# Optimization experiments

Measured on AMD Instinct MI355X. Metric: run time of the kernel, lower is better.

The kernel has to match this reference:

```python
import jax, jax.numpy as jnp
import numpy as np

N = 50000
E = 1600000
F_IN = 128
MP_UNITS = [32, 32, 32, 32, 16, 16, 16, 16, 8, 8, 8, 8]
MLP_UNITS = [16, 16]
DELTA = 2.0


def _lin(k, fi, fo):
    kw, kb = jax.random.split(k)
    s = 1.0 / np.sqrt(fi)
    W = jax.random.uniform(kw, (fi, fo), minval=-s, maxval=s, dtype=jnp.float32)
    b = jax.random.uniform(kb, (fo,), minval=-s, maxval=s, dtype=jnp.float32)
    return W, b


def setup_inputs() -> dict:
    key = jax.random.key(0)
    ks = jax.random.split(key, 64)
    inp = {}
    inp['x'] = jax.random.normal(ks[0], (N, F_IN), dtype=jnp.float32)
    inp['edge_index'] = jax.random.randint(ks[1], (2, E), 0, N, dtype=jnp.int32)
    inp['edge_weight'] = jax.random.uniform(ks[2], (E,), dtype=jnp.float32)
    inp['Wi'], inp['bi'] = _lin(ks[3], F_IN, F_IN)
    d = F_IN
    for i, u in enumerate(MP_UNITS):
        inp['Wc%d' % i], inp['bc%d' % i] = _lin(ks[4 + i], d, u)
        d = u
    for i, u in enumerate(MLP_UNITS):
        inp['Wm%d' % i], inp['bm%d' % i] = _lin(ks[20 + i], d, u)
        d = u
    inp['Wf'], inp['bf'] = _lin(ks[30], d, 1)
    return inp


def reference(x, edge_index, edge_weight, Wi, bi,
              Wc0, bc0, Wc1, bc1, Wc2, bc2, Wc3, bc3, Wc4, bc4, Wc5, bc5,
              Wc6, bc6, Wc7, bc7, Wc8, bc8, Wc9, bc9, Wc10, bc10, Wc11, bc11,
              Wm0, bm0, Wm1, bm1, Wf, bf):
    n = x.shape[0]
    src, dst = edge_index[0], edge_index[1]
    # delta_gcn_matrix: P = (1-delta) I + delta * D^{-1/2} A D^{-1/2}
    deg = jax.ops.segment_sum(edge_weight, dst, num_segments=n)
    dinv = jnp.where(deg > 0, jax.lax.rsqrt(jnp.maximum(deg, 1e-12)), 0.0)
    w = DELTA * dinv[src] * edge_weight * dinv[dst]  # [E]
    self_w = 1.0 - DELTA

    h = x @ Wi + bi

    def conv(h, W, b):
        hw = h @ W                                        # [N, out]
        msg = hw[src] * w[:, None]                        # gather + scale [E, out]
        agg = jax.ops.segment_sum(msg, dst, num_segments=n)  # scatter-add
        return agg + self_w * hw + b                      # fold in self-loops

    convs = [(Wc0, bc0), (Wc1, bc1), (Wc2, bc2), (Wc3, bc3), (Wc4, bc4), (Wc5, bc5),
             (Wc6, bc6), (Wc7, bc7), (Wc8, bc8), (Wc9, bc9), (Wc10, bc10), (Wc11, bc11)]
    for W, b in convs:
        h = jnp.tanh(conv(h, W, b))
    for W, b in [(Wm0, bm0), (Wm1, bm1)]:
        h = jax.nn.relu(h @ W + b)
    return jnp.tanh(h @ Wf + bf)  # [N, 1]
```

## Files before the change

### kernel.cpp

```cpp
#include <hip/hip_runtime.h>


constexpr int kN = 50000;
constexpr int kE = 1600000;
constexpr float kSelfW = -1.0f;
constexpr int kCAP = 72;
constexpr int PAD_N = 50048;
constexpr int kPROWS = PAD_N / 8;
constexpr int E4  = kE / 4;
constexpr int E4B = (E4 + 255) / 256;
constexpr int NBG = (kN + 255) / 256;

typedef int      v4i __attribute__((ext_vector_type(4)));
typedef float    v4f __attribute__((ext_vector_type(4)));
typedef _Float16 h8v __attribute__((ext_vector_type(8)));

__device__ __forceinline__ int rowmap(int r) {
  return (r & 7) * kPROWS + (r >> 3);
}
__device__ __forceinline__ unsigned packcw(int col, float w) {
  _Float16 h = (_Float16)w;
  unsigned short u;
  __builtin_memcpy(&u, &h, 2);
  return (unsigned)(unsigned short)col | ((unsigned)u << 16);
}
__device__ __forceinline__ float unpw(unsigned e) {
  unsigned short u = (unsigned short)(e >> 16);
  _Float16 h;
  __builtin_memcpy(&h, &u, 2);
  return (float)h;
}
__device__ __forceinline__ float fast_tanh(float x) {
  float t = __expf(2.0f * x);
  float r = __builtin_amdgcn_rcpf(t + 1.0f);
  return 1.0f - 2.0f * r;
}

__global__ __launch_bounds__(256)
void prep(int* __restrict__ cnt, const float* __restrict__ Wi,
          const float* __restrict__ bi, const float* __restrict__ Wc0,
          float* __restrict__ Weff, float* __restrict__ beff) {
  if (blockIdx.x < 49) {
    int i = blockIdx.x * 1024 + threadIdx.x * 4;
    if (i < PAD_N) *reinterpret_cast<int4*>(cnt + i) = make_int4(0, 0, 0, 0);
  } else {
    int idx = (blockIdx.x - 49) * 256 + threadIdx.x;
    if (idx >= 129 * 32) return;
    int r = idx >> 5, j = idx & 31;
    float acc = 0.0f;
    if (r < 128) {
      for (int k = 0; k < 128; ++k) acc += Wi[r * 128 + k] * Wc0[k * 32 + j];
      Weff[r * 32 + j] = acc;
    } else {
      for (int k = 0; k < 128; ++k) acc += bi[k] * Wc0[k * 32 + j];
      beff[j] = acc;
    }
  }
}

__global__ __launch_bounds__(256)
void cnt_rank_kernel(const int* __restrict__ dst, int* __restrict__ cnt,
                     int* __restrict__ rank, int e4) {
  int i = blockIdx.x * blockDim.x + threadIdx.x;
  if (i >= e4) return;
  int4 d = reinterpret_cast<const int4*>(dst)[i];
  int4 r;
  r.x = atomicAdd(&cnt[d.x], 1);
  r.y = atomicAdd(&cnt[d.y], 1);
  r.z = atomicAdd(&cnt[d.z], 1);
  r.w = atomicAdd(&cnt[d.w], 1);
  reinterpret_cast<int4*>(rank)[i] = r;
}

__global__ __launch_bounds__(256)
void gemm0(const float* __restrict__ X, const float* __restrict__ Weff,
           const float* __restrict__ beff, _Float16* __restrict__ Y, int n) {
  __shared__ float smem[4128];
  for (int idx = threadIdx.x; idx < 128 * 32; idx += 256) {
    int j = idx >> 7, k = idx & 127;
    smem[j * 128 + k] = Weff[k * 32 + j];
  }
  if (threadIdx.x < 32) smem[4096 + threadIdx.x] = beff[threadIdx.x];
  __syncthreads();
  int row = blockIdx.x * 256 + threadIdx.x;
  if (row >= n) return;
  float acc[32];
#pragma unroll
  for (int j = 0; j < 32; ++j) acc[j] = smem[4096 + j];
  const float4* xr = reinterpret_cast<const float4*>(X + (size_t)row * 128);
  const float4* Ws4 = reinterpret_cast<const float4*>(smem);
  for (int k4 = 0; k4 < 32; ++k4) {
    float4 a = xr[k4];
#pragma unroll
    for (int j = 0; j < 32; ++j) {
      float4 wv = Ws4[j * 32 + k4];
      acc[j] += a.x * wv.x + a.y * wv.y + a.z * wv.z + a.w * wv.w;
    }
  }
  h8v* yr = reinterpret_cast<h8v*>(Y + (size_t)row * 32);
#pragma unroll
  for (int j8 = 0; j8 < 4; ++j8) {
    h8v v;
#pragma unroll
    for (int q = 0; q < 8; ++q) v[q] = (_Float16)acc[8 * j8 + q];
    yr[j8] = v;
  }
}

__global__ __launch_bounds__(256)
void build_part(const int* __restrict__ src, const int* __restrict__ dst,
                const float* __restrict__ ew, const int* __restrict__ rank,
                unsigned* __restrict__ ecw, int e4) {
  int p = blockIdx.x & 7;
  int i = (blockIdx.x >> 3) * 256 + threadIdx.x;
  if (i >= e4) return;
  v4i sv = __builtin_nontemporal_load(reinterpret_cast<const v4i*>(src) + i);
  v4i dv = __builtin_nontemporal_load(reinterpret_cast<const v4i*>(dst) + i);
  v4i rv = __builtin_nontemporal_load(reinterpret_cast<const v4i*>(rank) + i);
  v4f wv = __builtin_nontemporal_load(reinterpret_cast<const v4f*>(ew) + i);
#pragma unroll
  for (int c = 0; c < 4; ++c) {
    int d = dv[c];
    if ((d & 7) == p) {
      int r = rv[c];
      if (r < kCAP)
        ecw[(size_t)(p * kPROWS + (d >> 3)) * kCAP + r] = packcw(sv[c], wv[c]);
    }
  }
}

__global__ __launch_bounds__(256)
void deg_dinv_wave(const int* __restrict__ cnt, const unsigned* __restrict__ ecw,
                   float* __restrict__ dinv, int n) {
  int lane = threadIdx.x & 63;
  int row = blockIdx.x * 4 + (threadIdx.x >> 6);
  int deg = min(cnt[row], kCAP);
  int base = rowmap(row) * kCAP;
  float d = 0.0f;
  for (int i = lane; i < deg; i += 64) d += unpw(ecw[base + i]);
#pragma unroll
  for (int off = 32; off > 0; off >>= 1) d += __shfl_xor(d, off, 64);
  if (lane == 0) dinv[row] = (d > 0.0f) ? rsqrtf(fmaxf(d, 1e-12f)) : 0.0f;
}

__global__ __launch_bounds__(256)
void wscale_wave(const int* __restrict__ cnt, unsigned* __restrict__ ecw,
                 const float* __restrict__ dinv, int n) {
  int lane = threadIdx.x & 63;
  int row = blockIdx.x * 4 + (threadIdx.x >> 6);
  int deg = min(cnt[row], kCAP);
  int base = rowmap(row) * kCAP;
  float dr = 2.0f * dinv[row];
  for (int i = lane; i < kCAP; i += 64) {
    if (i < deg) {
      unsigned e = ecw[base + i];
      int col = e & 0xFFFFu;
      ecw[base + i] = packcw(col, dr * dinv[col] * unpw(e));
    } else {
      ecw[base + i] = 0u;
    }
  }
}

template <int DOUT, int DNEXT, bool FINAL>
__global__ __launch_bounds__(256)
void spmm_fused(const _Float16* __restrict__ HW, const int* __restrict__ cnt,
                const unsigned* __restrict__ ecw, const float* __restrict__ b,
                const float* __restrict__ Wn, void* __restrict__ Out,
                const float* __restrict__ Wm0, const float* __restrict__ bm0,
                const float* __restrict__ Wm1, const float* __restrict__ bm1,
                const float* __restrict__ Wf, const float* __restrict__ bf,
                int n) {
  constexpr int R = 32 / DOUT;
  constexpr int W = 64 / R;
  constexpr int L = DOUT / 8;
  constexpr int S = W / L;
  constexpr int WST = DNEXT + 1;
  __shared__ float smem[(DNEXT > 0) ? DOUT * WST : 448];
  if constexpr (DNEXT > 0) {
    for (int idx = threadIdx.x; idx < DOUT * DNEXT; idx += 256) {
      int k = idx / DNEXT, j = idx - k * DNEXT;
      smem[k * WST + j] = Wn[idx];
    }
    __syncthreads();
  }
  if constexpr (FINAL) {
    int t = threadIdx.x;
    if (t < 128) smem[t] = Wm0[t];
    if (t < 256) smem[128 + t] = Wm1[t];
    if (t < 16) {
      smem[384 + t] = bm0[t];
      smem[400 + t] = bm1[t];
      smem[416 + t] = Wf[t];
    }
    if (t == 0) smem[432] = bf[0];
    __syncthreads();
  }
  int lane = threadIdx.x & 63;
  int wid = threadIdx.x >> 6;
  int g = lane / W;
  int gl = lane - g * W;
  int ch8 = gl & (L - 1);
  int sub = gl / L;
  int row = (blockIdx.x * 4 + wid) * R + g;
  int deg = min(cnt[row], kCAP);
  const uint4* ecw4 = reinterpret_cast<const uint4*>(ecw + rowmap(row) * kCAP);
  const h8v* HW8 = reinterpret_cast<const h8v*>(HW);
  uint4 ev = ecw4[sub];
  h8v hv0 = HW8[(size_t)(ev.x & 0xFFFFu) * L + ch8];
  h8v hv1 = HW8[(size_t)(ev.y & 0xFFFFu) * L + ch8];
  h8v hv2 = HW8[(size_t)(ev.z & 0xFFFFu) * L + ch8];
  h8v hv3 = HW8[(size_t)(ev.w & 0xFFFFu) * L + ch8];
  float w0 = unpw(ev.x), w1 = unpw(ev.y), w2 = unpw(ev.z), w3 = unpw(ev.w);
  float acc[8];
#pragma unroll
  for (int q = 0; q < 8; ++q)
    acc[q] = w0 * (float)hv0[q] + w1 * (float)hv1[q] +
             w2 * (float)hv2[q] + w3 * (float)hv3[q];
  if (deg > 64) {
    if (sub < 2) {
      uint4 et = ecw4[16 + sub];
      h8v t0 = HW8[(size_t)(et.x & 0xFFFFu) * L + ch8];
      h8v t1 = HW8[(size_t)(et.y & 0xFFFFu) * L + ch8];
      h8v t2 = HW8[(size_t)(et.z & 0xFFFFu) * L + ch8];
      h8v t3 = HW8[(size_t)(et.w & 0xFFFFu) * L + ch8];
      float u0 = unpw(et.x), u1 = unpw(et.y), u2 = unpw(et.z), u3 = unpw(et.w);
#pragma unroll
      for (int q = 0; q < 8; ++q)
        acc[q] += u0 * (float)t0[q] + u1 * (float)t1[q] +
                  u2 * (float)t2[q] + u3 * (float)t3[q];
    }
  }
#pragma unroll
  for (int off = W / 2; off >= L; off >>= 1) {
#pragma unroll
    for (int q = 0; q < 8; ++q) acc[q] += __shfl_xor(acc[q], off, 64);
  }
  int krow = 8 * ch8;
  h8v hsv = HW8[(size_t)row * L + ch8];
  float h[8];
#pragma unroll
  for (int q = 0; q < 8; ++q)
    h[q] = fast_tanh(acc[q] + kSelfW * (float)hsv[q] + b[krow + q]);
  if constexpr (FINAL) {
    if (gl == 0) {
      float y0[16];
#pragma unroll
      for (int j = 0; j < 16; ++j) {
        float v = smem[384 + j];
#pragma unroll
        for (int k = 0; k < 8; ++k) v += h[k] * smem[k * 16 + j];
        y0[j] = fmaxf(v, 0.0f);
      }
      float y1[16];
#pragma unroll
      for (int j = 0; j < 16; ++j) {
        float v = smem[400 + j];
#pragma unroll
        for (int k = 0; k < 16; ++k) v += y0[k] * smem[128 + k * 16 + j];
        y1[j] = fmaxf(v, 0.0f);
      }
      float z = smem[432];
#pragma unroll
      for (int k = 0; k < 16; ++k) z += y1[k] * smem[416 + k];
      reinterpret_cast<float*>(Out)[row] = fast_tanh(z);
    }
  } else {
    constexpr int JPT = (DNEXT >= S) ? (DNEXT / S) : 1;
    int jbase = (DNEXT >= S) ? sub * JPT : (sub & (DNEXT - 1));
    float pj[JPT];
#pragma unroll
    for (int jj = 0; jj < JPT; ++jj) {
      int j = jbase + jj;
      float v = 0.0f;
#pragma unroll
      for (int q = 0; q < 8; ++q) v += h[q] * smem[(krow + q) * WST + j];
      pj[jj] = v;
    }
#pragma unroll
    for (int off = 1; off < L; off <<= 1) {
#pragma unroll
      for (int jj = 0; jj < JPT; ++jj) pj[jj] += __shfl_xor(pj[jj], off, 64);
    }
    if (ch8 == 0 && (DNEXT >= S || sub < DNEXT)) {
      _Float16* op = reinterpret_cast<_Float16*>(Out) + (size_t)row * DNEXT + jbase;
      if constexpr (JPT == 2) {
        _Float16 a0 = (_Float16)pj[0], a1 = (_Float16)pj[1];
        unsigned short u0, u1;
        __builtin_memcpy(&u0, &a0, 2);
        __builtin_memcpy(&u1, &a1, 2);
        unsigned u = (unsigned)u0 | ((unsigned)u1 << 16);
        *reinterpret_cast<unsigned*>(op) = u;
      } else {
        op[0] = (_Float16)pj[0];
      }
    }
  }
}

extern "C" void kernel_launch(void* const* d_in, const int* in_sizes, int n_in,
                              void* d_out, int out_size, void* d_ws, size_t ws_size,
                              hipStream_t stream) {
  const float* x   = (const float*)d_in[0];
  const int*  eidx = (const int*)d_in[1];
  const float* ew  = (const float*)d_in[2];
  const float* Wi  = (const float*)d_in[3];
  const float* bi  = (const float*)d_in[4];
  const float* Wc[12]; const float* bc[12];
  for (int i = 0; i < 12; ++i) {
    Wc[i] = (const float*)d_in[5 + 2 * i];
    bc[i] = (const float*)d_in[6 + 2 * i];
  }
  const float* Wm0 = (const float*)d_in[29]; const float* bm0 = (const float*)d_in[30];
  const float* Wm1 = (const float*)d_in[31]; const float* bm1 = (const float*)d_in[32];
  const float* Wf  = (const float*)d_in[33]; const float* bf  = (const float*)d_in[34];
  float* out = (float*)d_out;

  const int* src = eidx;
  const int* dst = eidx + kE;

  float* wsf = (float*)d_ws;
  size_t off = 0;
  float*     dinv = wsf + off;              off += PAD_N;
  float*     Weff = wsf + off;              off += 128 * 32;
  float*     beff = wsf + off;              off += 64;
  int*       cnt  = (int*)(wsf + off);      off += PAD_N;
  unsigned*  ecw  = (unsigned*)(wsf + off); off += (size_t)PAD_N * kCAP;
  int*       rank = (int*)(wsf + off);      off += kE;
  _Float16*  B16  = (_Float16*)(wsf + off); off += (size_t)kN * 16;
  _Float16*  C16  = (_Float16*)(wsf + off); off += (size_t)kN * 16;

  const int sb32 = kN / 4;
  const int sb16 = kN / 8;
  const int sb8  = kN / 16;

  prep<<<66, 256, 0, stream>>>(cnt, Wi, bi, Wc[0], Weff, beff);
  cnt_rank_kernel<<<E4B, 256, 0, stream>>>(dst, cnt, rank, E4);
  gemm0<<<NBG, 256, 0, stream>>>(x, Weff, beff, B16, kN);
  build_part<<<E4B * 8, 256, 0, stream>>>(src, dst, ew, rank, ecw, E4);
  deg_dinv_wave<<<sb32, 256, 0, stream>>>(cnt, ecw, dinv, kN);
  wscale_wave<<<sb32, 256, 0, stream>>>(cnt, ecw, dinv, kN);

  spmm_fused<32, 32, false><<<sb32, 256, 0, stream>>>(B16, cnt, ecw, bc[0], Wc[1], C16, nullptr, nullptr, nullptr, nullptr, nullptr, nullptr, kN);
  spmm_fused<32, 32, false><<<sb32, 256, 0, stream>>>(C16, cnt, ecw, bc[1], Wc[2], B16, nullptr, nullptr, nullptr, nullptr, nullptr, nullptr, kN);
  spmm_fused<32, 32, false><<<sb32, 256, 0, stream>>>(B16, cnt, ecw, bc[2], Wc[3], C16, nullptr, nullptr, nullptr, nullptr, nullptr, nullptr, kN);
  spmm_fused<32, 16, false><<<sb32, 256, 0, stream>>>(C16, cnt, ecw, bc[3], Wc[4], B16, nullptr, nullptr, nullptr, nullptr, nullptr, nullptr, kN);
  spmm_fused<16, 16, false><<<sb16, 256, 0, stream>>>(B16, cnt, ecw, bc[4], Wc[5], C16, nullptr, nullptr, nullptr, nullptr, nullptr, nullptr, kN);
  spmm_fused<16, 16, false><<<sb16, 256, 0, stream>>>(C16, cnt, ecw, bc[5], Wc[6], B16, nullptr, nullptr, nullptr, nullptr, nullptr, nullptr, kN);
  spmm_fused<16, 16, false><<<sb16, 256, 0, stream>>>(B16, cnt, ecw, bc[6], Wc[7], C16, nullptr, nullptr, nullptr, nullptr, nullptr, nullptr, kN);
  spmm_fused<16, 8, false><<<sb16, 256, 0, stream>>>(C16, cnt, ecw, bc[7], Wc[8], B16, nullptr, nullptr, nullptr, nullptr, nullptr, nullptr, kN);
  spmm_fused<8, 8, false><<<sb8, 256, 0, stream>>>(B16, cnt, ecw, bc[8], Wc[9], C16, nullptr, nullptr, nullptr, nullptr, nullptr, nullptr, kN);
  spmm_fused<8, 8, false><<<sb8, 256, 0, stream>>>(C16, cnt, ecw, bc[9], Wc[10], B16, nullptr, nullptr, nullptr, nullptr, nullptr, nullptr, kN);
  spmm_fused<8, 8, false><<<sb8, 256, 0, stream>>>(B16, cnt, ecw, bc[10], Wc[11], C16, nullptr, nullptr, nullptr, nullptr, nullptr, nullptr, kN);
  spmm_fused<8, 0, true><<<sb8, 256, 0, stream>>>(C16, cnt, ecw, bc[11], nullptr, out, Wm0, bm0, Wm1, bm1, Wf, bf, kN);
}
```

Baseline: 557.8 us.

## Use persistent grid-stride SpMM blocks with register-held weights and 2-edge loads

```diff
diff --git a/kernel.cpp b/kernel.cpp
--- a/kernel.cpp
+++ b/kernel.cpp
@@ -10,6 +10,7 @@
 constexpr int E4  = kE / 4;
 constexpr int E4B = (E4 + 255) / 256;
 constexpr int NBG = (kN + 255) / 256;
+constexpr int SB  = 2048;
 
 typedef int      v4i __attribute__((ext_vector_type(4)));
 typedef float    v4f __attribute__((ext_vector_type(4)));
@@ -175,15 +176,8 @@
   constexpr int W = 64 / R;
   constexpr int L = DOUT / 8;
   constexpr int S = W / L;
-  constexpr int WST = DNEXT + 1;
-  __shared__ float smem[(DNEXT > 0) ? DOUT * WST : 448];
-  if constexpr (DNEXT > 0) {
-    for (int idx = threadIdx.x; idx < DOUT * DNEXT; idx += 256) {
-      int k = idx / DNEXT, j = idx - k * DNEXT;
-      smem[k * WST + j] = Wn[idx];
-    }
-    __syncthreads();
-  }
+  constexpr int JPT = (DNEXT > 0) ? ((DNEXT >= S) ? (DNEXT / S) : 1) : 1;
+  __shared__ float smem[FINAL ? 448 : 1];
   if constexpr (FINAL) {
     int t = threadIdx.x;
     if (t < 128) smem[t] = Wm0[t];
@@ -202,97 +196,112 @@
   int gl = lane - g * W;
   int ch8 = gl & (L - 1);
   int sub = gl / L;
-  int row = (blockIdx.x * 4 + wid) * R + g;
-  int deg = min(cnt[row], kCAP);
-  const uint4* ecw4 = reinterpret_cast<const uint4*>(ecw + rowmap(row) * kCAP);
+  int krow = 8 * ch8;
+  int jbase = 0;
+  float WsR[JPT][8];
+  if constexpr (DNEXT > 0) {
+    jbase = (DNEXT >= S) ? sub * JPT : (sub & (DNEXT - 1));
+#pragma unroll
+    for (int jj = 0; jj < JPT; ++jj)
+#pragma unroll
+      for (int q = 0; q < 8; ++q)
+        WsR[jj][q] = Wn[(krow + q) * DNEXT + jbase + jj];
+  }
+  float bR[8];
+#pragma unroll
+  for (int q = 0; q < 8; ++q) bR[q] = b[krow + q];
   const h8v* HW8 = reinterpret_cast<const h8v*>(HW);
-  uint4 ev = ecw4[sub];
-  h8v hv0 = HW8[(size_t)(ev.x & 0xFFFFu) * L + ch8];
-  h8v hv1 = HW8[(size_t)(ev.y & 0xFFFFu) * L + ch8];
-  h8v hv2 = HW8[(size_t)(ev.z & 0xFFFFu) * L + ch8];
-  h8v hv3 = HW8[(size_t)(ev.w & 0xFFFFu) * L + ch8];
-  float w0 = unpw(ev.x), w1 = unpw(ev.y), w2 = unpw(ev.z), w3 = unpw(ev.w);
-  float acc[8];
-#pragma unroll
-  for (int q = 0; q < 8; ++q)
-    acc[q] = w0 * (float)hv0[q] + w1 * (float)hv1[q] +
-             w2 * (float)hv2[q] + w3 * (float)hv3[q];
-  if (deg > 64) {
-    if (sub < 2) {
-      uint4 et = ecw4[16 + sub];
-      h8v t0 = HW8[(size_t)(et.x & 0xFFFFu) * L + ch8];
-      h8v t1 = HW8[(size_t)(et.y & 0xFFFFu) * L + ch8];
-      h8v t2 = HW8[(size_t)(et.z & 0xFFFFu) * L + ch8];
-      h8v t3 = HW8[(size_t)(et.w & 0xFFFFu) * L + ch8];
-      float u0 = unpw(et.x), u1 = unpw(et.y), u2 = unpw(et.z), u3 = unpw(et.w);
+  const int stride = SB * 4 * R;
+  for (int row = (blockIdx.x * 4 + wid) * R + g; row < n; row += stride) {
+    int deg = min(cnt[row], kCAP);
+    const uint2* ecw2 = reinterpret_cast<const uint2*>(ecw + rowmap(row) * kCAP);
+    uint2 ea = ecw2[sub];
+    h8v ha0 = HW8[(size_t)(ea.x & 0xFFFFu) * L + ch8];
+    h8v ha1 = HW8[(size_t)(ea.y & 0xFFFFu) * L + ch8];
+    float wa0 = unpw(ea.x), wa1 = unpw(ea.y);
+    float acc[8];
+#pragma unroll
+    for (int q = 0; q < 8; ++q)
+      acc[q] = wa0 * (float)ha0[q] + wa1 * (float)ha1[q];
+    if (deg > 32) {
+      uint2 eb = ecw2[16 + sub];
+      h8v hb0 = HW8[(size_t)(eb.x & 0xFFFFu) * L + ch8];
+      h8v hb1 = HW8[(size_t)(eb.y & 0xFFFFu) * L + ch8];
+      float wb0 = unpw(eb.x), wb1 = unpw(eb.y);
 #pragma unroll
       for (int q = 0; q < 8; ++q)
-        acc[q] += u0 * (float)t0[q] + u1 * (float)t1[q] +
-                  u2 * (float)t2[q] + u3 * (float)t3[q];
-    }
-  }
-#pragma unroll
-  for (int off = W / 2; off >= L; off >>= 1) {
-#pragma unroll
-    for (int q = 0; q < 8; ++q) acc[q] += __shfl_xor(acc[q], off, 64);
-  }
-  int krow = 8 * ch8;
-  h8v hsv = HW8[(size_t)row * L + ch8];
-  float h[8];
-#pragma unroll
-  for (int q = 0; q < 8; ++q)
-    h[q] = fast_tanh(acc[q] + kSelfW * (float)hsv[q] + b[krow + q]);
-  if constexpr (FINAL) {
-    if (gl == 0) {
-      float y0[16];
-#pragma unroll
-      for (int j = 0; j < 16; ++j) {
-        float v = smem[384 + j];
-#pragma unroll
-        for (int k = 0; k < 8; ++k) v += h[k] * smem[k * 16 + j];
-        y0[j] = fmaxf(v, 0.0f);
-      }
-      float y1[16];
-#pragma unroll
-      for (int j = 0; j < 16; ++j) {
-        float v = smem[400 + j];
-#pragma unroll
-        for (int k = 0; k < 16; ++k) v += y0[k] * smem[128 + k * 16 + j];
-        y1[j] = fmaxf(v, 0.0f);
-      }
-      float z = smem[432];
-#pragma unroll
-      for (int k = 0; k < 16; ++k) z += y1[k] * smem[416 + k];
-      reinterpret_cast<float*>(Out)[row] = fast_tanh(z);
-    }
-  } else {
-    constexpr int JPT = (DNEXT >= S) ? (DNEXT / S) : 1;
-    int jbase = (DNEXT >= S) ? sub * JPT : (sub & (DNEXT - 1));
-    float pj[JPT];
-#pragma unroll
-    for (int jj = 0; jj < JPT; ++jj) {
-      int j = jbase + jj;
-      float v = 0.0f;
-#pragma unroll
-      for (int q = 0; q < 8; ++q) v += h[q] * smem[(krow + q) * WST + j];
-      pj[jj] = v;
-    }
-#pragma unroll
-    for (int off = 1; off < L; off <<= 1) {
-#pragma unroll
-      for (int jj = 0; jj < JPT; ++jj) pj[jj] += __shfl_xor(pj[jj], off, 64);
-    }
-    if (ch8 == 0 && (DNEXT >= S || sub < DNEXT)) {
-      _Float16* op = reinterpret_cast<_Float16*>(Out) + (size_t)row * DNEXT + jbase;
-      if constexpr (JPT == 2) {
-        _Float16 a0 = (_Float16)pj[0], a1 = (_Float16)pj[1];
-        unsigned short u0, u1;
-        __builtin_memcpy(&u0, &a0, 2);
-        __builtin_memcpy(&u1, &a1, 2);
-        unsigned u = (unsigned)u0 | ((unsigned)u1 << 16);
-        *reinterpret_cast<unsigned*>(op) = u;
-      } else {
-        op[0] = (_Float16)pj[0];
+        acc[q] += wb0 * (float)hb0[q] + wb1 * (float)hb1[q];
+    }
+    if (deg > 64) {
+      if (sub < 4) {
+        uint2 et = ecw2[32 + sub];
+        h8v t0 = HW8[(size_t)(et.x & 0xFFFFu) * L + ch8];
+        h8v t1 = HW8[(size_t)(et.y & 0xFFFFu) * L + ch8];
+        float u0 = unpw(et.x), u1 = unpw(et.y);
+#pragma unroll
+        for (int q = 0; q < 8; ++q)
+          acc[q] += u0 * (float)t0[q] + u1 * (float)t1[q];
+      }
+    }
+#pragma unroll
+    for (int off = W / 2; off >= L; off >>= 1) {
+#pragma unroll
+      for (int q = 0; q < 8; ++q) acc[q] += __shfl_xor(acc[q], off, 64);
+    }
+    h8v hsv = HW8[(size_t)row * L + ch8];
+    float h[8];
+#pragma unroll
+    for (int q = 0; q < 8; ++q)
+      h[q] = fast_tanh(acc[q] + kSelfW * (float)hsv[q] + bR[q]);
+    if constexpr (FINAL) {
+      if (gl == 0) {
+        float y0[16];
+#pragma unroll
+        for (int j = 0; j < 16; ++j) {
+          float v = smem[384 + j];
+#pragma unroll
+          for (int k = 0; k < 8; ++k) v += h[k] * smem[k * 16 + j];
+          y0[j] = fmaxf(v, 0.0f);
+        }
+        float y1[16];
+#pragma unroll
+        for (int j = 0; j < 16; ++j) {
+          float v = smem[400 + j];
+#pragma unroll
+          for (int k = 0; k < 16; ++k) v += y0[k] * smem[128 + k * 16 + j];
+          y1[j] = fmaxf(v, 0.0f);
+        }
+        float z = smem[432];
+#pragma unroll
+        for (int k = 0; k < 16; ++k) z += y1[k] * smem[416 + k];
+        reinterpret_cast<float*>(Out)[row] = fast_tanh(z);
+      }
+    } else {
+      float pj[JPT];
+#pragma unroll
+      for (int jj = 0; jj < JPT; ++jj) {
+        float v = 0.0f;
+#pragma unroll
+        for (int q = 0; q < 8; ++q) v += h[q] * WsR[jj][q];
+        pj[jj] = v;
+      }
+#pragma unroll
+      for (int off = 1; off < L; off <<= 1) {
+#pragma unroll
+        for (int jj = 0; jj < JPT; ++jj) pj[jj] += __shfl_xor(pj[jj], off, 64);
+      }
+      if (ch8 == 0 && (DNEXT >= S || sub < DNEXT)) {
+        _Float16* op = reinterpret_cast<_Float16*>(Out) + (size_t)row * DNEXT + jbase;
+        if constexpr (JPT == 2) {
+          _Float16 a0 = (_Float16)pj[0], a1 = (_Float16)pj[1];
+          unsigned short u0, u1;
+          __builtin_memcpy(&u0, &a0, 2);
+          __builtin_memcpy(&u1, &a1, 2);
+          unsigned u = (unsigned)u0 | ((unsigned)u1 << 16);
+          *reinterpret_cast<unsigned*>(op) = u;
+        } else {
+          op[0] = (_Float16)pj[0];
+        }
       }
     }
   }
@@ -331,8 +340,6 @@
   _Float16*  C16  = (_Float16*)(wsf + off); off += (size_t)kN * 16;
 
   const int sb32 = kN / 4;
-  const int sb16 = kN / 8;
-  const int sb8  = kN / 16;
 
   prep<<<66, 256, 0, stream>>>(cnt, Wi, bi, Wc[0], Weff, beff);
   cnt_rank_kernel<<<E4B, 256, 0, stream>>>(dst, cnt, rank, E4);
@@ -341,16 +348,16 @@
   deg_dinv_wave<<<sb32, 256, 0, stream>>>(cnt, ecw, dinv, kN);
   wscale_wave<<<sb32, 256, 0, stream>>>(cnt, ecw, dinv, kN);
 
-  spmm_fused<32, 32, false><<<sb32, 256, 0, stream>>>(B16, cnt, ecw, bc[0], Wc[1], C16, nullptr, nullptr, nullptr, nullptr, nullptr, nullptr, kN);
-  spmm_fused<32, 32, false><<<sb32, 256, 0, stream>>>(C16, cnt, ecw, bc[1], Wc[2], B16, nullptr, nullptr, nullptr, nullptr, nullptr, nullptr, kN);
-  spmm_fused<32, 32, false><<<sb32, 256, 0, stream>>>(B16, cnt, ecw, bc[2], Wc[3], C16, nullptr, nullptr, nullptr, nullptr, nullptr, nullptr, kN);
-  spmm_fused<32, 16, false><<<sb32, 256, 0, stream>>>(C16, cnt, ecw, bc[3], Wc[4], B16, nullptr, nullptr, nullptr, nullptr, nullptr, nullptr, kN);
-  spmm_fused<16, 16, false><<<sb16, 256, 0, stream>>>(B16, cnt, ecw, bc[4], Wc[5], C16, nullptr, nullptr, nullptr, nullptr, nullptr, nullptr, kN);
-  spmm_fused<16, 16, false><<<sb16, 256, 0, stream>>>(C16, cnt, ecw, bc[5], Wc[6], B16, nullptr, nullptr, nullptr, nullptr, nullptr, nullptr, kN);
-  spmm_fused<16, 16, false><<<sb16, 256, 0, stream>>>(B16, cnt, ecw, bc[6], Wc[7], C16, nullptr, nullptr, nullptr, nullptr, nullptr, nullptr, kN);
-  spmm_fused<16, 8, false><<<sb16, 256, 0, stream>>>(C16, cnt, ecw, bc[7], Wc[8], B16, nullptr, nullptr, nullptr, nullptr, nullptr, nullptr, kN);
-  spmm_fused<8, 8, false><<<sb8, 256, 0, stream>>>(B16, cnt, ecw, bc[8], Wc[9], C16, nullptr, nullptr, nullptr, nullptr, nullptr, nullptr, kN);
-  spmm_fused<8, 8, false><<<sb8, 256, 0, stream>>>(C16, cnt, ecw, bc[9], Wc[10], B16, nullptr, nullptr, nullptr, nullptr, nullptr, nullptr, kN);
-  spmm_fused<8, 8, false><<<sb8, 256, 0, stream>>>(B16, cnt, ecw, bc[10], Wc[11], C16, nullptr, nullptr, nullptr, nullptr, nullptr, nullptr, kN);
-  spmm_fused<8, 0, true><<<sb8, 256, 0, stream>>>(C16, cnt, ecw, bc[11], nullptr, out, Wm0, bm0, Wm1, bm1, Wf, bf, kN);
-}
+  spmm_fused<32, 32, false><<<SB, 256, 0, stream>>>(B16, cnt, ecw, bc[0], Wc[1], C16, nullptr, nullptr, nullptr, nullptr, nullptr, nullptr, kN);
+  spmm_fused<32, 32, false><<<SB, 256, 0, stream>>>(C16, cnt, ecw, bc[1], Wc[2], B16, nullptr, nullptr, nullptr, nullptr, nullptr, nullptr, kN);
+  spmm_fused<32, 32, false><<<SB, 256, 0, stream>>>(B16, cnt, ecw, bc[2], Wc[3], C16, nullptr, nullptr, nullptr, nullptr, nullptr, nullptr, kN);
+  spmm_fused<32, 16, false><<<SB, 256, 0, stream>>>(C16, cnt, ecw, bc[3], Wc[4], B16, nullptr, nullptr, nullptr, nullptr, nullptr, nullptr, kN);
+  spmm_fused<16, 16, false><<<SB, 256, 0, stream>>>(B16, cnt, ecw, bc[4], Wc[5], C16, nullptr, nullptr, nullptr, nullptr, nullptr, nullptr, kN);
+  spmm_fused<16, 16, false><<<SB, 256, 0, stream>>>(C16, cnt, ecw, bc[5], Wc[6], B16, nullptr, nullptr, nullptr, nullptr, nullptr, nullptr, kN);
+  spmm_fused<16, 16, false><<<SB, 256, 0, stream>>>(B16, cnt, ecw, bc[6], Wc[7], C16, nullptr, nullptr, nullptr, nullptr, nullptr, nullptr, kN);
+  spmm_fused<16, 8, false><<<SB, 256, 0, stream>>>(C16, cnt, ecw, bc[7], Wc[8], B16, nullptr, nullptr, nullptr, nullptr, nullptr, nullptr, kN);
+  spmm_fused<8, 8, false><<<SB, 256, 0, stream>>>(B16, cnt, ecw, bc[8], Wc[9], C16, nullptr, nullptr, nullptr, nullptr, nullptr, nullptr, kN);
+  spmm_fused<8, 8, false><<<SB, 256, 0, stream>>>(C16, cnt, ecw, bc[9], Wc[10], B16, nullptr, nullptr, nullptr, nullptr, nullptr, nullptr, kN);
+  spmm_fused<8, 8, false><<<SB, 256, 0, stream>>>(B16, cnt, ecw, bc[10], Wc[11], C16, nullptr, nullptr, nullptr, nullptr, nullptr, nullptr, kN);
+  spmm_fused<8, 0, true><<<SB, 256, 0, stream>>>(C16, cnt, ecw, bc[11], nullptr, out, Wm0, bm0, Wm1, bm1, Wf, bf, kN);
+}
```

New measurement: 621.1 us. 11.4% more time.

## Halve lanes per row in SpMM so each wave handles twice the rows

Applied to the files above, without the earlier changes.

```diff
diff --git a/kernel.cpp b/kernel.cpp
--- a/kernel.cpp
+++ b/kernel.cpp
@@ -10,6 +10,7 @@
 constexpr int E4  = kE / 4;
 constexpr int E4B = (E4 + 255) / 256;
 constexpr int NBG = (kN + 255) / 256;
+constexpr int WSN = 50016;
 
 typedef int      v4i __attribute__((ext_vector_type(4)));
 typedef float    v4f __attribute__((ext_vector_type(4)));
@@ -29,6 +30,13 @@
   _Float16 h;
   __builtin_memcpy(&h, &u, 2);
   return (float)h;
+}
+__device__ __forceinline__ unsigned pack2h(float a, float b) {
+  _Float16 ha = (_Float16)a, hb = (_Float16)b;
+  unsigned short ua, ub;
+  __builtin_memcpy(&ua, &ha, 2);
+  __builtin_memcpy(&ub, &hb, 2);
+  return (unsigned)ua | ((unsigned)ub << 16);
 }
 __device__ __forceinline__ float fast_tanh(float x) {
   float t = __expf(2.0f * x);
@@ -148,6 +156,7 @@
                  const float* __restrict__ dinv, int n) {
   int lane = threadIdx.x & 63;
   int row = blockIdx.x * 4 + (threadIdx.x >> 6);
+  if (row >= n) return;
   int deg = min(cnt[row], kCAP);
   int base = rowmap(row) * kCAP;
   float dr = 2.0f * dinv[row];
@@ -171,11 +180,12 @@
                 const float* __restrict__ Wm1, const float* __restrict__ bm1,
                 const float* __restrict__ Wf, const float* __restrict__ bf,
                 int n) {
-  constexpr int R = 32 / DOUT;
-  constexpr int W = 64 / R;
+  constexpr int R = 64 / DOUT;
+  constexpr int W = DOUT;
   constexpr int L = DOUT / 8;
-  constexpr int S = W / L;
+  constexpr int S = 8;
   constexpr int WST = DNEXT + 1;
+  constexpr int JPT = (DNEXT > 0) ? (DNEXT / S) : 1;
   __shared__ float smem[(DNEXT > 0) ? DOUT * WST : 448];
   if constexpr (DNEXT > 0) {
     for (int idx = threadIdx.x; idx < DOUT * DNEXT; idx += 256) {
@@ -206,17 +216,25 @@
   int deg = min(cnt[row], kCAP);
   const uint4* ecw4 = reinterpret_cast<const uint4*>(ecw + rowmap(row) * kCAP);
   const h8v* HW8 = reinterpret_cast<const h8v*>(HW);
-  uint4 ev = ecw4[sub];
-  h8v hv0 = HW8[(size_t)(ev.x & 0xFFFFu) * L + ch8];
-  h8v hv1 = HW8[(size_t)(ev.y & 0xFFFFu) * L + ch8];
-  h8v hv2 = HW8[(size_t)(ev.z & 0xFFFFu) * L + ch8];
-  h8v hv3 = HW8[(size_t)(ev.w & 0xFFFFu) * L + ch8];
-  float w0 = unpw(ev.x), w1 = unpw(ev.y), w2 = unpw(ev.z), w3 = unpw(ev.w);
+  uint4 ea = ecw4[sub];
+  uint4 eb = ecw4[8 + sub];
+  h8v a0 = HW8[(size_t)(ea.x & 0xFFFFu) * L + ch8];
+  h8v a1 = HW8[(size_t)(ea.y & 0xFFFFu) * L + ch8];
+  h8v a2 = HW8[(size_t)(ea.z & 0xFFFFu) * L + ch8];
+  h8v a3 = HW8[(size_t)(ea.w & 0xFFFFu) * L + ch8];
+  h8v b0 = HW8[(size_t)(eb.x & 0xFFFFu) * L + ch8];
+  h8v b1 = HW8[(size_t)(eb.y & 0xFFFFu) * L + ch8];
+  h8v b2 = HW8[(size_t)(eb.z & 0xFFFFu) * L + ch8];
+  h8v b3 = HW8[(size_t)(eb.w & 0xFFFFu) * L + ch8];
+  float wa0 = unpw(ea.x), wa1 = unpw(ea.y), wa2 = unpw(ea.z), wa3 = unpw(ea.w);
+  float wb0 = unpw(eb.x), wb1 = unpw(eb.y), wb2 = unpw(eb.z), wb3 = unpw(eb.w);
   float acc[8];
 #pragma unroll
   for (int q = 0; q < 8; ++q)
-    acc[q] = w0 * (float)hv0[q] + w1 * (float)hv1[q] +
-             w2 * (float)hv2[q] + w3 * (float)hv3[q];
+    acc[q] = wa0 * (float)a0[q] + wa1 * (float)a1[q] +
+             wa2 * (float)a2[q] + wa3 * (float)a3[q] +
+             wb0 * (float)b0[q] + wb1 * (float)b1[q] +
+             wb2 * (float)b2[q] + wb3 * (float)b3[q];
   if (deg > 64) {
     if (sub < 2) {
       uint4 et = ecw4[16 + sub];
@@ -243,7 +261,7 @@
   for (int q = 0; q < 8; ++q)
     h[q] = fast_tanh(acc[q] + kSelfW * (float)hsv[q] + b[krow + q]);
   if constexpr (FINAL) {
-    if (gl == 0) {
+    if (gl == 0 && row < n) {
       float y0[16];
 #pragma unroll
       for (int j = 0; j < 16; ++j) {
@@ -266,9 +284,8 @@
       reinterpret_cast<float*>(Out)[row] = fast_tanh(z);
     }
   } else {
-    constexpr int JPT = (DNEXT >= S) ? (DNEXT / S) : 1;
-    int jbase = (DNEXT >= S) ? sub * JPT : (sub & (DNEXT - 1));
     float pj[JPT];
+    int jbase = sub * JPT;
 #pragma unroll
     for (int jj = 0; jj < JPT; ++jj) {
       int j = jbase + jj;
@@ -282,15 +299,13 @@
 #pragma unroll
       for (int jj = 0; jj < JPT; ++jj) pj[jj] += __shfl_xor(pj[jj], off, 64);
     }
-    if (ch8 == 0 && (DNEXT >= S || sub < DNEXT)) {
+    if (ch8 == 0 && row < n) {
       _Float16* op = reinterpret_cast<_Float16*>(Out) + (size_t)row * DNEXT + jbase;
-      if constexpr (JPT == 2) {
-        _Float16 a0 = (_Float16)pj[0], a1 = (_Float16)pj[1];
-        unsigned short u0, u1;
-        __builtin_memcpy(&u0, &a0, 2);
-        __builtin_memcpy(&u1, &a1, 2);
-        unsigned u = (unsigned)u0 | ((unsigned)u1 << 16);
-        *reinterpret_cast<unsigned*>(op) = u;
+      if constexpr (JPT == 4) {
+        uint2 u = make_uint2(pack2h(pj[0], pj[1]), pack2h(pj[2], pj[3]));
+        *reinterpret_cast<uint2*>(op) = u;
+      } else if constexpr (JPT == 2) {
+        *reinterpret_cast<unsigned*>(op) = pack2h(pj[0], pj[1]);
       } else {
         op[0] = (_Float16)pj[0];
       }
@@ -330,16 +345,18 @@
   _Float16*  B16  = (_Float16*)(wsf + off); off += (size_t)kN * 16;
   _Float16*  C16  = (_Float16*)(wsf + off); off += (size_t)kN * 16;
 
-  const int sb32 = kN / 4;
-  const int sb16 = kN / 8;
-  const int sb8  = kN / 16;
+  const int dgb  = kN / 4;
+  const int wsb  = WSN / 4;
+  const int sb32 = kN / 8;
+  const int sb16 = kN / 16;
+  const int sb8  = (kN + 31) / 32;
 
   prep<<<66, 256, 0, stream>>>(cnt, Wi, bi, Wc[0], Weff, beff);
   cnt_rank_kernel<<<E4B, 256, 0, stream>>>(dst, cnt, rank, E4);
   gemm0<<<NBG, 256, 0, stream>>>(x, Weff, beff, B16, kN);
   build_part<<<E4B * 8, 256, 0, stream>>>(src, dst, ew, rank, ecw, E4);
-  deg_dinv_wave<<<sb32, 256, 0, stream>>>(cnt, ecw, dinv, kN);
-  wscale_wave<<<sb32, 256, 0, stream>>>(cnt, ecw, dinv, kN);
+  deg_dinv_wave<<<dgb, 256, 0, stream>>>(cnt, ecw, dinv, kN);
+  wscale_wave<<<wsb, 256, 0, stream>>>(cnt, ecw, dinv, WSN);
 
   spmm_fused<32, 32, false><<<sb32, 256, 0, stream>>>(B16, cnt, ecw, bc[0], Wc[1], C16, nullptr, nullptr, nullptr, nullptr, nullptr, nullptr, kN);
   spmm_fused<32, 32, false><<<sb32, 256, 0, stream>>>(C16, cnt, ecw, bc[1], Wc[2], B16, nullptr, nullptr, nullptr, nullptr, nullptr, nullptr, kN);
```

New measurement: 531.4 us. -4.7%, faster.
